# Optimization experiments

Measured on AMD Instinct MI355X. Metric: run time of the kernel, lower is better.

The kernel has to match this reference:

```python
import jax, jax.numpy as jnp
import numpy as np

N_HEAD = 16
N_KV_HEADS = 4
N_REP = 4
HEAD_DIM = 128
N_EMBD = 2048
EPS = 1e-5
ROPE_BASE = 10000.0


def setup_inputs() -> dict:
    key = jax.random.key(0)
    ks = jax.random.split(key, 5)
    B, T, C = 2, 2048, N_EMBD
    s = 0.02
    return {
        "x": jax.random.normal(ks[0], (B, T, C), dtype=jnp.float32),
        "wq": jax.random.normal(ks[1], (C, N_HEAD * HEAD_DIM), dtype=jnp.float32) * s,
        "wk": jax.random.normal(ks[2], (C, N_KV_HEADS * HEAD_DIM), dtype=jnp.float32) * s,
        "wv": jax.random.normal(ks[3], (C, N_KV_HEADS * HEAD_DIM), dtype=jnp.float32) * s,
        "wc": jax.random.normal(ks[4], (C, C), dtype=jnp.float32) * s,
        "q_norm_w": jnp.ones((HEAD_DIM,), dtype=jnp.float32),
        "k_norm_w": jnp.ones((HEAD_DIM,), dtype=jnp.float32),
    }


def _rmsnorm(x, w):
    # norm in fp32, scale by weight (matches RMSNorm.forward)
    xf = x.astype(jnp.float32)
    rms = jax.lax.rsqrt(jnp.mean(xf * xf, axis=-1, keepdims=True) + EPS)
    return (xf * rms).astype(x.dtype) * w


def _rope(x, cos, sin):
    # x: [B,T,H,D]; cos/sin: [T, D//2]; interleaved even/odd rotation
    xf = x.astype(jnp.float32)
    xe = xf[..., 0::2]
    xo = xf[..., 1::2]
    c = cos[None, :, None, :]
    s = sin[None, :, None, :]
    ye = xe * c - xo * s
    yo = xe * s + xo * c
    y = jnp.stack((ye, yo), axis=-1).reshape(x.shape)
    return y.astype(x.dtype)


def reference(x, wq, wk, wv, wc, q_norm_w, k_norm_w):
    B, T, C = x.shape
    q = (x @ wq).reshape(B, T, N_HEAD, HEAD_DIM)
    k = (x @ wk).reshape(B, T, N_KV_HEADS, HEAD_DIM)
    v = (x @ wv).reshape(B, T, N_KV_HEADS, HEAD_DIM)

    q = _rmsnorm(q, q_norm_w)
    k = _rmsnorm(k, k_norm_w)

    inv_freq = 1.0 / (ROPE_BASE ** (jnp.arange(0, HEAD_DIM, 2, dtype=jnp.float32) / HEAD_DIM))
    theta = jnp.arange(T, dtype=jnp.float32)[:, None] * inv_freq[None, :]  # [T, D//2]
    cos, sin = jnp.cos(theta), jnp.sin(theta)
    q = _rope(q, cos, sin)
    k = _rope(k, cos, sin)

    # GQA: repeat kv heads (repeat_kv with n_rep)
    k = jnp.repeat(k, N_REP, axis=2)  # [B,T,H,D]
    v = jnp.repeat(v, N_REP, axis=2)

    scale = 1.0 / jnp.sqrt(jnp.float32(HEAD_DIM))
    scores = jnp.einsum("bthd,bshd->bhts", q, k) * scale  # [B,H,T,S]
    causal = jnp.tril(jnp.ones((T, T), dtype=bool))
    scores = jnp.where(causal[None, None], scores, jnp.finfo(scores.dtype).min)
    attn = jax.nn.softmax(scores, axis=-1)
    y = jnp.einsum("bhts,bshd->bthd", attn, v).reshape(B, T, C)
    return y @ wc
```

## Files before the change

kernel.cpp:

```cpp
#include <hip/hip_runtime.h>
#include <hip/hip_bf16.h>
#include <cstdint>
#include <cstddef>

using bf16 = __hip_bfloat16;
typedef __attribute__((ext_vector_type(8))) short short8;
typedef __attribute__((ext_vector_type(4))) float f32x4;
typedef __attribute__((ext_vector_type(16))) float f32x16;

#define T_SEQ 2048
#define NHEAD 16
#define NKV 4
#define HD 128
#define CE 2048

__device__ __forceinline__ void gl_lds16(const void* g, void* l) {
  __builtin_amdgcn_global_load_lds(
      (const __attribute__((address_space(1))) unsigned int*)g,
      (__attribute__((address_space(3))) unsigned int*)l, 16, 0, 0);
}

__device__ __forceinline__ unsigned int cvtpk_bf16(float lo, float hi) {
  unsigned int r;
  asm("v_cvt_pk_bf16_f32 %0, %1, %2" : "=v"(r) : "v"(lo), "v"(hi));
  return r;
}

__device__ __forceinline__ void plswap(unsigned int& x, unsigned int& y, int hi) {
#if __has_builtin(__builtin_amdgcn_permlane32_swap)
  auto r = __builtin_amdgcn_permlane32_swap(x, y, false, false);
  x = r[0];
  y = r[1];
#else
  unsigned int xp = (unsigned int)__shfl_xor((int)x, 32);
  unsigned int yp = (unsigned int)__shfl_xor((int)y, 32);
  unsigned int nx = hi ? yp : x;
  unsigned int ny = hi ? y : xp;
  x = nx;
  y = ny;
#endif
}

__global__ void __launch_bounds__(256) cvt_bf16(const float* __restrict__ in,
                                                bf16* __restrict__ out, int n4) {
  const int i = blockIdx.x * blockDim.x + threadIdx.x;
  if (i >= n4) return;
  const float4 v = ((const float4*)in)[i];
  bf16 b0 = __float2bfloat16(v.x), b1 = __float2bfloat16(v.y),
       b2 = __float2bfloat16(v.z), b3 = __float2bfloat16(v.w);
  ushort4 u;
  u.x = *(const unsigned short*)&b0; u.y = *(const unsigned short*)&b1;
  u.z = *(const unsigned short*)&b2; u.w = *(const unsigned short*)&b3;
  ((ushort4*)out)[i] = u;
}

__global__ void __launch_bounds__(256) transpose_cvt(const float* __restrict__ W,
                                                     bf16* __restrict__ Wt, int N) {
  __shared__ float tile[32][33];
  const int tx = threadIdx.x & 31, ty = threadIdx.x >> 5;
  const int bx = blockIdx.x, by = blockIdx.y;
#pragma unroll
  for (int i = 0; i < 4; i++) {
    const int r = by * 32 + ty + i * 8;
    tile[ty + i * 8][tx] = W[(size_t)r * N + bx * 32 + tx];
  }
  __syncthreads();
#pragma unroll
  for (int i = 0; i < 4; i++) {
    const int n = bx * 32 + ty + i * 8;
    Wt[(size_t)n * 2048 + by * 32 + tx] = __float2bfloat16(tile[tx][ty + i * 8]);
  }
}

__global__ void __launch_bounds__(256) gemm_bt(const bf16* __restrict__ A,
                                               const bf16* __restrict__ Bt,
                                               float* __restrict__ C,
                                               int M, int N, int K) {
  __shared__ bf16 smA[128 * 64];
  __shared__ bf16 smB[128 * 64];
  const int tid = threadIdx.x, wid = tid >> 6, lane = tid & 63;
  const int l15 = lane & 15, l4 = lane >> 4;
  const int l8 = lane >> 3, l7 = lane & 7;
  const int row0 = blockIdx.y * 128, col0 = blockIdx.x * 128;
  const int wm = wid >> 1, wn = wid & 1;
  const int gcol = (l7 ^ l8) * 8;

  f32x4 acc[4][4];
#pragma unroll
  for (int m = 0; m < 4; m++)
#pragma unroll
    for (int n = 0; n < 4; n++) acc[m][n] = (f32x4){0.f, 0.f, 0.f, 0.f};

  const bf16* Ab = A + (size_t)row0 * K + gcol;
  const bf16* Bb = Bt + (size_t)col0 * K + gcol;

  for (int k0 = 0; k0 < K; k0 += 64) {
    __syncthreads();
#pragma unroll
    for (int i = 0; i < 4; i++) {
      const int c = wid * 4 + i;
      const int r = c * 8 + l8;
      gl_lds16(Ab + (size_t)r * K + k0, (void*)(smA + c * 512));
      gl_lds16(Bb + (size_t)r * K + k0, (void*)(smB + c * 512));
    }
    __syncthreads();
#pragma unroll
    for (int kc = 0; kc < 2; kc++) {
      short8 af[4], bfr[4];
#pragma unroll
      for (int m = 0; m < 4; m++) {
        const int r = wm * 64 + m * 16 + l15;
        af[m] = *(const short8*)(smA + r * 64 + ((((kc << 2) | l4) ^ (r & 7)) * 8));
      }
#pragma unroll
      for (int n = 0; n < 4; n++) {
        const int r = wn * 64 + n * 16 + l15;
        bfr[n] = *(const short8*)(smB + r * 64 + ((((kc << 2) | l4) ^ (r & 7)) * 8));
      }
#pragma unroll
      for (int m = 0; m < 4; m++)
#pragma unroll
        for (int n = 0; n < 4; n++)
          acc[m][n] = __builtin_amdgcn_mfma_f32_16x16x32_bf16(af[m], bfr[n], acc[m][n], 0, 0, 0);
    }
  }
#pragma unroll
  for (int m = 0; m < 4; m++)
#pragma unroll
    for (int n = 0; n < 4; n++)
#pragma unroll
      for (int r = 0; r < 4; r++)
        C[(size_t)(row0 + wm * 64 + m * 16 + l4 * 4 + r) * N +
          (col0 + wn * 64 + n * 16 + l15)] = acc[m][n][r];
}

__global__ void __launch_bounds__(256) qkv_post(const float* __restrict__ QKV,
                                                const float* __restrict__ qw,
                                                const float* __restrict__ kw,
                                                bf16* __restrict__ Qo,
                                                bf16* __restrict__ Ko,
                                                bf16* __restrict__ Vto) {
  const int g = blockIdx.x * 4 + (threadIdx.x >> 6);
  const int lane = threadIdx.x & 63;
  const int hh = g % 24;
  const int bt = g / 24;
  const int b = bt >> 11, t = bt & (T_SEQ - 1);
  int off;
  if (hh < 16) off = hh * 128;
  else if (hh < 20) off = 2048 + (hh - 16) * 128;
  else off = 2560 + (hh - 20) * 128;
  const float2 x = *(const float2*)(QKV + (size_t)bt * 3072 + off + lane * 2);
  if (hh < 20) {
    float ss = x.x * x.x + x.y * x.y;
    ss += __shfl_xor(ss, 1);  ss += __shfl_xor(ss, 2);  ss += __shfl_xor(ss, 4);
    ss += __shfl_xor(ss, 8);  ss += __shfl_xor(ss, 16); ss += __shfl_xor(ss, 32);
    const float rms = rsqrtf(ss * (1.0f / 128.0f) + 1e-5f);
    const float* w = (hh < 16) ? qw : kw;
    const float x0 = x.x * rms * w[lane * 2];
    const float x1 = x.y * rms * w[lane * 2 + 1];
    const float inv = exp2f((float)lane * (-13.287712379549449f / 64.0f));
    const float th = (float)t * inv;
    const float sn = sinf(th), cs = cosf(th);
    const float y0 = x0 * cs - x1 * sn;
    const float y1 = x0 * sn + x1 * cs;
    const bf16 o0 = __float2bfloat16(y0), o1 = __float2bfloat16(y1);
    if (hh < 16) {
      bf16* d = Qo + ((size_t)(b * NHEAD + hh) * T_SEQ + t) * HD + lane * 2;
      d[0] = o0; d[1] = o1;
    } else {
      bf16* d = Ko + ((size_t)(b * NKV + (hh - 16)) * T_SEQ + t) * HD + lane * 2;
      d[0] = o0; d[1] = o1;
    }
  } else {
    bf16* d = Vto + ((size_t)(b * NKV + (hh - 20)) * HD + lane * 2) * T_SEQ + t;
    d[0] = __float2bfloat16(x.x);
    d[T_SEQ] = __float2bfloat16(x.y);
  }
}

__global__ void __launch_bounds__(256, 2) attn_fwd(const bf16* __restrict__ Q,
                                                   const bf16* __restrict__ K,
                                                   const bf16* __restrict__ Vt,
                                                   bf16* __restrict__ Y) {
  __shared__ bf16 smK[128 * 128];
  __shared__ bf16 smV[128 * 128];

  const int bid = blockIdx.x;
  const int p = bid & 255, sdx = bid >> 8;
  const int bh = p & 31;
  const int jh = p >> 5;
  const int jq = sdx ? (15 - jh) : jh;
  const int h = bh & (NHEAD - 1), b = bh >> 4;
  const int bkv = b * NKV + (h >> 2);

  const int tid = threadIdx.x, wid = tid >> 6, lane = tid & 63;
  const int l31 = lane & 31, hi = lane >> 5;
  const int bq0 = jq * 128;
  const int q0w = bq0 + wid * 32;

  const bf16* Kb = K + (size_t)bkv * T_SEQ * HD;
  const bf16* Vb = Vt + (size_t)bkv * HD * T_SEQ;

  const bf16* Qrow = Q + ((size_t)bh * T_SEQ + q0w + l31) * HD + hi * 8;
  short8 qf[8];
#pragma unroll
  for (int ds = 0; ds < 8; ds++) qf[ds] = *(const short8*)(Qrow + ds * 16);

  f32x16 o[4];
#pragma unroll
  for (int d = 0; d < 4; d++) o[d] = (f32x16)(0.f);
  float mrun = -INFINITY, lrun = 0.f;

  constexpr float CL = 0.08838834764831845f * 1.44269504088896340736f;
  const int trow = tid >> 4, tslot = tid & 15;

  for (int t = 0; t <= jq; t++) {
    const int k0 = t * 128;
    __syncthreads();
#pragma unroll
    for (int i = 0; i < 8; i++) {
      const int row = i * 16 + trow;
      const int ss = (tslot ^ (row & 15)) * 8;
      gl_lds16(Kb + (size_t)(k0 + row) * HD + ss, (void*)((char*)smK + i * 4096 + wid * 1024));
      gl_lds16(Vb + (size_t)row * T_SEQ + k0 + ss, (void*)((char*)smV + i * 4096 + wid * 1024));
    }
    __syncthreads();

    const bool lastt = (t == jq);
    const int glim = lastt ? wid : 3;

    f32x16 sg[4];
#pragma unroll
    for (int g = 0; g < 4; g++) {
      if (g > glim) continue;
      f32x16 acc = (f32x16)(0.f);
#pragma unroll
      for (int ds = 0; ds < 8; ds++) {
        const int row = g * 32 + l31;
        const short8 kf = *(const short8*)(smK + (size_t)row * 128 +
                                           (((ds << 1) | hi) ^ (row & 15)) * 8);
        acc = __builtin_amdgcn_mfma_f32_32x32x16_bf16(kf, qf[ds], acc, 0, 0, 0);
      }
      sg[g] = acc;
    }
    float tmax = -INFINITY;
#pragma unroll
    for (int g = 0; g < 4; g++) {
      if (g > glim) continue;
      if (lastt && g == wid) {
#pragma unroll
        for (int r = 0; r < 16; r++) {
          const int kr = (r & 3) + 8 * (r >> 2) + (hi << 2);
          if (kr > l31) sg[g][r] = -INFINITY;
        }
      }
#pragma unroll
      for (int r = 0; r < 16; r++) tmax = fmaxf(tmax, sg[g][r]);
    }
    tmax = fmaxf(tmax, __shfl_xor(tmax, 32));
    const float mnew = fmaxf(mrun, tmax);
    const float f = exp2f((mrun - mnew) * CL);
    mrun = mnew;
    lrun *= f;
#pragma unroll
    for (int d = 0; d < 4; d++)
#pragma unroll
      for (int r = 0; r < 16; r++) o[d][r] *= f;

    float lsum = 0.f;
#pragma unroll
    for (int g = 0; g < 4; g++) {
      if (g > glim) continue;
      float pp[16];
      float s0 = 0.f, s1 = 0.f;
#pragma unroll
      for (int r = 0; r < 16; r++) pp[r] = exp2f((sg[g][r] - mnew) * CL);
#pragma unroll
      for (int r = 0; r < 8; r++) { s0 += pp[2 * r]; s1 += pp[2 * r + 1]; }
      lsum += s0 + s1;

      unsigned int w0 = cvtpk_bf16(pp[0], pp[1]),  w2 = cvtpk_bf16(pp[4], pp[5]);
      unsigned int w1 = cvtpk_bf16(pp[2], pp[3]),  w3 = cvtpk_bf16(pp[6], pp[7]);
      unsigned int w4 = cvtpk_bf16(pp[8], pp[9]),  w6 = cvtpk_bf16(pp[12], pp[13]);
      unsigned int w5 = cvtpk_bf16(pp[10], pp[11]), w7 = cvtpk_bf16(pp[14], pp[15]);
      plswap(w0, w2, hi); plswap(w1, w3, hi);
      plswap(w4, w6, hi); plswap(w5, w7, hi);
      union { unsigned int u[4]; short8 s8; } pa0, pa1;
      pa0.u[0] = w0; pa0.u[1] = w1; pa0.u[2] = w2; pa0.u[3] = w3;
      pa1.u[0] = w4; pa1.u[1] = w5; pa1.u[2] = w6; pa1.u[3] = w7;

#pragma unroll
      for (int d = 0; d < 4; d++) {
        const int row = d * 32 + l31;
        const int ks0 = g * 2, ks1 = g * 2 + 1;
        const short8 vf0 = *(const short8*)(smV + (size_t)row * 128 +
                                            (((ks0 << 1) | hi) ^ (row & 15)) * 8);
        const short8 vf1 = *(const short8*)(smV + (size_t)row * 128 +
                                            (((ks1 << 1) | hi) ^ (row & 15)) * 8);
        o[d] = __builtin_amdgcn_mfma_f32_32x32x16_bf16(vf0, pa0.s8, o[d], 0, 0, 0);
        o[d] = __builtin_amdgcn_mfma_f32_32x32x16_bf16(vf1, pa1.s8, o[d], 0, 0, 0);
      }
    }
    lrun += lsum + __shfl_xor(lsum, 32);
  }

  const float inv = 1.0f / lrun;
  bf16* yrow = Y + ((size_t)(b * T_SEQ + q0w + l31)) * CE + h * HD;
#pragma unroll
  for (int d = 0; d < 4; d++) {
#pragma unroll
    for (int rg = 0; rg < 4; rg++) {
      ushort4 u;
      bf16 e0 = __float2bfloat16(o[d][rg * 4 + 0] * inv);
      bf16 e1 = __float2bfloat16(o[d][rg * 4 + 1] * inv);
      bf16 e2 = __float2bfloat16(o[d][rg * 4 + 2] * inv);
      bf16 e3 = __float2bfloat16(o[d][rg * 4 + 3] * inv);
      u.x = *(const unsigned short*)&e0; u.y = *(const unsigned short*)&e1;
      u.z = *(const unsigned short*)&e2; u.w = *(const unsigned short*)&e3;
      *(ushort4*)(yrow + d * 32 + rg * 8 + (hi << 2)) = u;
    }
  }
}

extern "C" void kernel_launch(void* const* d_in, const int* in_sizes, int n_in,
                              void* d_out, int out_size, void* d_ws, size_t ws_size,
                              hipStream_t stream) {
  const float* x   = (const float*)d_in[0];
  const float* wq  = (const float*)d_in[1];
  const float* wk  = (const float*)d_in[2];
  const float* wv  = (const float*)d_in[3];
  const float* wc  = (const float*)d_in[4];
  const float* qnw = (const float*)d_in[5];
  const float* knw = (const float*)d_in[6];
  float* out = (float*)d_out;

  char* ws = (char*)d_ws;
  bf16*  xb    = (bf16*)(ws);
  bf16*  wqkvt = (bf16*)(ws + 16777216);
  bf16*  wct   = (bf16*)(ws + 29360128);
  float* qkv   = (float*)(ws + 37748736);
  bf16*  Qb    = (bf16*)(ws + 88080384);
  bf16*  Kb    = (bf16*)(ws + 104857600);
  bf16*  Vtb   = (bf16*)(ws + 109051904);
  bf16*  yb    = (bf16*)(ws + 113246208);

  cvt_bf16<<<8192, 256, 0, stream>>>(x, xb, 2097152);
  transpose_cvt<<<dim3(64, 64), 256, 0, stream>>>(wq, wqkvt, 2048);
  transpose_cvt<<<dim3(16, 64), 256, 0, stream>>>(wk, wqkvt + (size_t)2048 * 2048, 512);
  transpose_cvt<<<dim3(16, 64), 256, 0, stream>>>(wv, wqkvt + (size_t)2560 * 2048, 512);
  transpose_cvt<<<dim3(64, 64), 256, 0, stream>>>(wc, wct, 2048);
  gemm_bt<<<dim3(24, 32), 256, 0, stream>>>(xb, wqkvt, qkv, 4096, 3072, 2048);
  qkv_post<<<24576, 256, 0, stream>>>(qkv, qnw, knw, Qb, Kb, Vtb);
  attn_fwd<<<512, 256, 0, stream>>>(Qb, Kb, Vtb, yb);
  gemm_bt<<<dim3(16, 32), 256, 0, stream>>>(yb, wct, out, 4096, 2048, 2048);
}
```

Measured before the change: 241.1 us.

## Replace GEMM with double-buffered 8-wave pipelined kernel and XCD-aware tile mapping

Replaces the single-buffered 128x128 bf16 GEMM with a templated 512-thread kernel using larger tiles (256x256 for QKV, 256x128 for output projection). Global-to-LDS loads are double-buffered and interleaved with quarter-tile MFMA phases separated by barriers, with s_setprio raised around the MFMA blocks. Workgroup IDs are remapped so contiguous tiles land on the same XCD for L2 reuse. The aim is to hide memory latency and raise MFMA utilisation, at the cost of fewer workgroups (192/256) and more register and LDS pressure per block.

```diff
diff --git a/kernel.cpp b/kernel.cpp
--- a/kernel.cpp
+++ b/kernel.cpp
@@ -72,66 +72,133 @@
   }
 }
 
-__global__ void __launch_bounds__(256) gemm_bt(const bf16* __restrict__ A,
-                                               const bf16* __restrict__ Bt,
-                                               float* __restrict__ C,
-                                               int M, int N, int K) {
-  __shared__ bf16 smA[128 * 64];
-  __shared__ bf16 smB[128 * 64];
-  const int tid = threadIdx.x, wid = tid >> 6, lane = tid & 63;
+#define LOADA(mh)                                                              \
+  _Pragma("unroll") for (int i = 0; i < MF / 2; i++) {                         \
+    const int lrow = wr * (BM / WM) + ((mh) * (MF / 2) + i) * 16 + l15;        \
+    _Pragma("unroll") for (int kk = 0; kk < 2; kk++) {                         \
+      areg[i][kk] = *(const short8*)(sA + lrow * 64 +                          \
+                    ((((kk << 2) | l4) ^ (lrow & 7)) << 3));                   \
+    }                                                                          \
+  }
+
+#define LOADB(nh)                                                              \
+  _Pragma("unroll") for (int j = 0; j < NF / 2; j++) {                         \
+    const int lrow = wc * (BN / WN) + ((nh) * (NF / 2) + j) * 16 + l15;        \
+    _Pragma("unroll") for (int kk = 0; kk < 2; kk++) {                         \
+      breg[j][kk] = *(const short8*)(sB + lrow * 64 +                          \
+                    ((((kk << 2) | l4) ^ (lrow & 7)) << 3));                   \
+    }                                                                          \
+  }
+
+#define MFMAQ(mh, nh)                                                          \
+  __builtin_amdgcn_s_setprio(1);                                               \
+  _Pragma("unroll") for (int i = 0; i < MF / 2; i++)                           \
+  _Pragma("unroll") for (int j = 0; j < NF / 2; j++)                           \
+  _Pragma("unroll") for (int kk = 0; kk < 2; kk++)                             \
+    acc[(mh) * (MF / 2) + i][(nh) * (NF / 2) + j] =                            \
+        __builtin_amdgcn_mfma_f32_16x16x32_bf16(                               \
+            areg[i][kk], breg[j][kk],                                          \
+            acc[(mh) * (MF / 2) + i][(nh) * (NF / 2) + j], 0, 0, 0);           \
+  __builtin_amdgcn_s_setprio(0);
+
+template <int BM, int BN, int WM, int WN>
+__global__ void __launch_bounds__(512, 2)
+gemm8p(const bf16* __restrict__ A, const bf16* __restrict__ Bt,
+       float* __restrict__ C, int M, int N, int K) {
+  constexpr int MF = BM / WM / 16;
+  constexpr int NF = BN / WN / 16;
+  constexpr int AL = BM / 64;
+  constexpr int BL = BN / 64;
+  __shared__ bf16 smA[2][BM * 64];
+  __shared__ bf16 smB[2][BN * 64];
+
+  const int tid = threadIdx.x, lane = tid & 63, wid = tid >> 6;
   const int l15 = lane & 15, l4 = lane >> 4;
-  const int l8 = lane >> 3, l7 = lane & 7;
-  const int row0 = blockIdx.y * 128, col0 = blockIdx.x * 128;
-  const int wm = wid >> 1, wn = wid & 1;
-  const int gcol = (l7 ^ l8) * 8;
-
-  f32x4 acc[4][4];
-#pragma unroll
-  for (int m = 0; m < 4; m++)
-#pragma unroll
-    for (int n = 0; n < 4; n++) acc[m][n] = (f32x4){0.f, 0.f, 0.f, 0.f};
-
-  const bf16* Ab = A + (size_t)row0 * K + gcol;
-  const bf16* Bb = Bt + (size_t)col0 * K + gcol;
-
-  for (int k0 = 0; k0 < K; k0 += 64) {
-    __syncthreads();
-#pragma unroll
-    for (int i = 0; i < 4; i++) {
-      const int c = wid * 4 + i;
-      const int r = c * 8 + l8;
-      gl_lds16(Ab + (size_t)r * K + k0, (void*)(smA + c * 512));
-      gl_lds16(Bb + (size_t)r * K + k0, (void*)(smB + c * 512));
-    }
-    __syncthreads();
-#pragma unroll
-    for (int kc = 0; kc < 2; kc++) {
-      short8 af[4], bfr[4];
-#pragma unroll
-      for (int m = 0; m < 4; m++) {
-        const int r = wm * 64 + m * 16 + l15;
-        af[m] = *(const short8*)(smA + r * 64 + ((((kc << 2) | l4) ^ (r & 7)) * 8));
-      }
-#pragma unroll
-      for (int n = 0; n < 4; n++) {
-        const int r = wn * 64 + n * 16 + l15;
-        bfr[n] = *(const short8*)(smB + r * 64 + ((((kc << 2) | l4) ^ (r & 7)) * 8));
-      }
-#pragma unroll
-      for (int m = 0; m < 4; m++)
-#pragma unroll
-        for (int n = 0; n < 4; n++)
-          acc[m][n] = __builtin_amdgcn_mfma_f32_16x16x32_bf16(af[m], bfr[n], acc[m][n], 0, 0, 0);
-    }
-  }
-#pragma unroll
-  for (int m = 0; m < 4; m++)
-#pragma unroll
-    for (int n = 0; n < 4; n++)
-#pragma unroll
-      for (int r = 0; r < 4; r++)
-        C[(size_t)(row0 + wm * 64 + m * 16 + l4 * 4 + r) * N +
-          (col0 + wn * 64 + n * 16 + l15)] = acc[m][n][r];
+  const int wr = wid / WN, wc = wid % WN;
+
+  const int nwg = gridDim.x;
+  const int q = nwg >> 3, r = nwg & 7;
+  const int xcd = blockIdx.x & 7, lin = blockIdx.x >> 3;
+  const int wg = (xcd < r ? xcd * (q + 1) : r * (q + 1) + (xcd - r) * q) + lin;
+  const int gw = N / BN;
+  const int by = wg / gw, bx = wg % gw;
+  const int row0 = by * BM, col0 = bx * BN;
+  const int NT = K >> 6;
+
+  const bf16* Ag = A + (size_t)row0 * K;
+  const bf16* Bg = Bt + (size_t)col0 * K;
+
+  auto stageA = [&](int t, int pbuf) {
+    const int k0 = t << 6;
+#pragma unroll
+    for (int j = 0; j < AL; j++) {
+      const int c = j * 512 + tid;
+      const int rowi = c >> 3;
+      gl_lds16(Ag + (size_t)rowi * K + k0 + (((c & 7) ^ (rowi & 7)) << 3),
+               (void*)(&smA[pbuf][c << 3]));
+    }
+  };
+  auto stageB = [&](int t, int pbuf) {
+    const int k0 = t << 6;
+#pragma unroll
+    for (int j = 0; j < BL; j++) {
+      const int c = j * 512 + tid;
+      const int rowi = c >> 3;
+      gl_lds16(Bg + (size_t)rowi * K + k0 + (((c & 7) ^ (rowi & 7)) << 3),
+               (void*)(&smB[pbuf][c << 3]));
+    }
+  };
+
+  f32x4 acc[MF][NF];
+#pragma unroll
+  for (int i = 0; i < MF; i++)
+#pragma unroll
+    for (int j = 0; j < NF; j++) acc[i][j] = (f32x4){0.f, 0.f, 0.f, 0.f};
+  short8 areg[MF / 2][2], breg[NF / 2][2];
+
+  stageA(0, 0);
+  stageB(0, 0);
+  stageA(1, 1);
+  asm volatile("s_waitcnt vmcnt(%0)" ::"i"(AL) : "memory");
+  __builtin_amdgcn_s_barrier();
+
+  for (int t = 0; t < NT; ++t) {
+    const int buf = t & 1;
+    const bf16* sA = smA[buf];
+    const bf16* sB = smB[buf];
+    const int tB = (t + 1 < NT) ? t + 1 : NT - 1;
+    const int tA = (t + 2 < NT) ? t + 2 : NT - 1;
+
+    stageB(tB, buf ^ 1);
+    LOADA(0)
+    LOADB(0)
+    __builtin_amdgcn_s_barrier();
+    MFMAQ(0, 0)
+    __builtin_amdgcn_s_barrier();
+    LOADB(1)
+    __builtin_amdgcn_s_barrier();
+    MFMAQ(0, 1)
+    __builtin_amdgcn_s_barrier();
+    LOADA(1)
+    __builtin_amdgcn_s_barrier();
+    MFMAQ(1, 1)
+    __builtin_amdgcn_s_barrier();
+    stageA(tA, buf);
+    LOADB(0)
+    asm volatile("s_waitcnt vmcnt(%0)" ::"i"(AL) : "memory");
+    __builtin_amdgcn_s_barrier();
+    MFMAQ(1, 0)
+    __builtin_amdgcn_s_barrier();
+  }
+
+#pragma unroll
+  for (int i = 0; i < MF; i++)
+#pragma unroll
+    for (int j = 0; j < NF; j++)
+#pragma unroll
+      for (int rr = 0; rr < 4; rr++)
+        C[(size_t)(row0 + wr * (BM / WM) + i * 16 + l4 * 4 + rr) * N +
+          (col0 + wc * (BN / WN) + j * 16 + l15)] = acc[i][j][rr];
 }
 
 __global__ void __launch_bounds__(256) qkv_post(const float* __restrict__ QKV,
@@ -195,8 +262,7 @@
 
   const int tid = threadIdx.x, wid = tid >> 6, lane = tid & 63;
   const int l31 = lane & 31, hi = lane >> 5;
-  const int bq0 = jq * 128;
-  const int q0w = bq0 + wid * 32;
+  const int q0w = jq * 128 + wid * 32;
 
   const bf16* Kb = K + (size_t)bkv * T_SEQ * HD;
   const bf16* Vb = Vt + (size_t)bkv * HD * T_SEQ;
@@ -349,8 +415,8 @@
   transpose_cvt<<<dim3(16, 64), 256, 0, stream>>>(wk, wqkvt + (size_t)2048 * 2048, 512);
   transpose_cvt<<<dim3(16, 64), 256, 0, stream>>>(wv, wqkvt + (size_t)2560 * 2048, 512);
   transpose_cvt<<<dim3(64, 64), 256, 0, stream>>>(wc, wct, 2048);
-  gemm_bt<<<dim3(24, 32), 256, 0, stream>>>(xb, wqkvt, qkv, 4096, 3072, 2048);
+  gemm8p<256, 256, 2, 4><<<192, 512, 0, stream>>>(xb, wqkvt, qkv, 4096, 3072, 2048);
   qkv_post<<<24576, 256, 0, stream>>>(qkv, qnw, knw, Qb, Kb, Vtb);
   attn_fwd<<<512, 256, 0, stream>>>(Qb, Kb, Vtb, yb);
-  gemm_bt<<<dim3(16, 32), 256, 0, stream>>>(yb, wct, out, 4096, 2048, 2048);
-}
+  gemm8p<256, 128, 4, 2><<<256, 512, 0, stream>>>(yb, wct, out, 4096, 2048, 2048);
+}
```

Result: no change. 240.6 us (-0.2%).
